# Performance work log

Measured on AMD Instinct MI355X. Metric: run time of the kernel, lower is better.

## Reference

```python
import jax, jax.numpy as jnp
import numpy as np

B, S, K, N, G = 4, 2048, 4096, 11008, 128


def setup_inputs() -> dict:
    key = jax.random.key(0)
    k1, k2, k3 = jax.random.split(key, 3)
    x = jax.random.normal(k1, (B, S, K), dtype=jnp.float32)
    # packed int4 GPTQ weights: (K/8, N) int32, 8 nibbles per int32
    qweight = jax.random.randint(k2, (K // 8, N), 0, 2147483647, dtype=jnp.int32)
    # per-group scales: (K/G, N), small positive values
    scales = jax.random.uniform(k3, (K // G, N), dtype=jnp.float32) * 0.01 + 0.001
    return {"x": x, "qweight": qweight, "scales": scales, "group_size": G}


def _dequantize(qweight, scales, group_size):
    shifts = jnp.arange(0, 32, 4, dtype=jnp.int32)          # [8]
    w = (qweight[:, None, :] >> shifts[None, :, None]) & 15  # (K/8, 8, N)
    k = w.shape[0] * 8
    w = w.reshape(k, -1)                                     # (K, N) in [0, 15]
    gidx = jnp.arange(k) // group_size                       # (K,)
    # symmetric int4 dequant with per-group, per-output-channel scale
    return (w.astype(scales.dtype) - 8.0) * scales[gidx]     # (K, N)


def reference(x, qweight, scales, group_size):
    Wf = _dequantize(qweight, scales, group_size)            # (K, N)
    return jnp.einsum('bsk,kn->bsn', x, Wf)                  # (B, S, N)
```

## Files before the change

kernel.cpp:

```cpp
#include <hip/hip_runtime.h>
#include <cstdint>
#include <cstddef>

#define M_DIM 8192
#define K_DIM 4096
#define N_DIM 11008
#define NT    (K_DIM / 64)

typedef short bf16x8 __attribute__((ext_vector_type(8)));
typedef float f32x4  __attribute__((ext_vector_type(4)));
typedef unsigned short us8 __attribute__((ext_vector_type(8)));

__device__ __forceinline__ unsigned short f2bf(float f) {
  unsigned int u = __float_as_uint(f);
  u += 0x7FFFu + ((u >> 16) & 1u);
  return (unsigned short)(u >> 16);
}

__global__ __launch_bounds__(256) void cvt_x_kernel(const float* __restrict__ x,
                                                    unsigned short* __restrict__ xb) {
  const int i = blockIdx.x * 256 + threadIdx.x;
  const float4* x4 = (const float4*)x;
  float4 a = x4[(size_t)i * 2];
  float4 b = x4[(size_t)i * 2 + 1];
  us8 o;
  o[0] = f2bf(a.x); o[1] = f2bf(a.y); o[2] = f2bf(a.z); o[3] = f2bf(a.w);
  o[4] = f2bf(b.x); o[5] = f2bf(b.y); o[6] = f2bf(b.z); o[7] = f2bf(b.w);
  *(us8*)(xb + (size_t)i * 8) = o;
}

__global__ __launch_bounds__(256) void dequant_kernel(const int* __restrict__ qw,
                                                      const float* __restrict__ sc,
                                                      unsigned short* __restrict__ wt) {
  const int n0 = blockIdx.x * 64;
  const int k0 = blockIdx.y * 64;
  const int g  = blockIdx.y >> 1;
  __shared__ unsigned short lds[64 * 64];
  const int t = threadIdx.x;
  {
    const int kk_l = t >> 5;
    const int n_l  = (t & 31) * 2;
    const int2  q2 = *(const int2*)&qw[(k0 / 8 + kk_l) * N_DIM + n0 + n_l];
    const float2 s2 = *(const float2*)&sc[g * N_DIM + n0 + n_l];
    us8 o0, o1;
#pragma unroll
    for (int j = 0; j < 8; ++j) {
      o0[j] = f2bf((float)(((q2.x >> (4 * j)) & 15) - 8) * s2.x);
      o1[j] = f2bf((float)(((q2.y >> (4 * j)) & 15) - 8) * s2.y);
    }
    *(us8*)&lds[(n_l    ) * 64 + kk_l * 8] = o0;
    *(us8*)&lds[(n_l + 1) * 64 + kk_l * 8] = o1;
  }
  __syncthreads();
#pragma unroll
  for (int it = 0; it < 2; ++it) {
    const int idx = t + it * 256;
    const int n_l = idx >> 3;
    const int ch  = (idx & 7) * 8;
    *(us8*)&wt[(size_t)(n0 + n_l) * K_DIM + k0 + ch] = *(const us8*)&lds[n_l * 64 + ch];
  }
}

__global__ __launch_bounds__(512, 2) void gemm_kernel(const unsigned short* __restrict__ A,
                                                      const unsigned short* __restrict__ Bt,
                                                      float* __restrict__ C) {
  __shared__ unsigned short lds[8][8192];
  const int t    = threadIdx.x;
  const int wave = t >> 6;
  const int lane = t & 63;
  const int l15  = lane & 15;
  const int wr   = wave >> 2;
  const int wc   = wave & 3;

  const int bid = blockIdx.x;
  const int wg  = (bid & 7) * 172 + (bid >> 3);
  const int m0  = (wg / 43) * 256;
  const int n0  = (wg % 43) * 256;

  const int sq = (t & 3) ^ ((t >> 3) & 3);
  const unsigned short* gA = A  + (size_t)(m0 + (t >> 2)) * K_DIM + sq * 8;
  const unsigned short* gB = Bt + (size_t)(n0 + (t >> 2)) * K_DIM + sq * 8;

  const int sxo   = ((lane >> 4) ^ ((l15 >> 1) & 3)) << 3;
  const int aoffA = (wr * 128 + l15) * 32 + sxo;
  const int aoffB = (wc * 64  + l15) * 32 + sxo;

  auto stage = [&](const unsigned short* gbase, unsigned short* reg, int h, int tk) {
#pragma unroll
    for (int j = 0; j < 2; ++j) {
      __builtin_amdgcn_global_load_lds(
          (const __attribute__((address_space(1))) unsigned int*)(gbase + (size_t)j * 128 * K_DIM + tk * 64 + h * 32),
          (__attribute__((address_space(3))) unsigned int*)(reg + j * 4096 + t * 8),
          16, 0, 0);
    }
  };

  f32x4 acc[8][4] = {};

  stage(gA, &lds[0][0], 0, 0);
  stage(gB, &lds[4][0], 0, 0);
  stage(gA, &lds[1][0], 1, 0);
  stage(gB, &lds[5][0], 1, 0);
  stage(gA, &lds[2][0], 0, 1);
  stage(gB, &lds[6][0], 0, 1);
  asm volatile("s_waitcnt vmcnt(4)" ::: "memory");
  __builtin_amdgcn_s_barrier();

#pragma unroll 1
  for (int tk = 0; tk < NT; ++tk) {
    const int p = tk & 1;
    const unsigned short* Ah0 = &lds[p * 2 + 0][0];
    const unsigned short* Ah1 = &lds[p * 2 + 1][0];
    const unsigned short* Bh0 = &lds[4 + p * 2 + 0][0];
    const unsigned short* Bh1 = &lds[4 + p * 2 + 1][0];
    unsigned short* stA1 = &lds[(p ^ 1) * 2 + 1][0];
    unsigned short* stB1 = &lds[4 + (p ^ 1) * 2 + 1][0];
    unsigned short* stA2 = &lds[p * 2 + 0][0];
    unsigned short* stB2 = &lds[4 + p * 2 + 0][0];

    bf16x8 a[4], b[4], a2[4];

#pragma unroll
    for (int i = 0; i < 4; ++i) a[i] = *(const bf16x8*)&Ah0[aoffA + i * 512];
#pragma unroll
    for (int i = 0; i < 4; ++i) b[i] = *(const bf16x8*)&Bh0[aoffB + i * 512];
    if (tk + 1 < NT) stage(gA, stA1, 1, tk + 1);
    __builtin_amdgcn_s_barrier();
    __builtin_amdgcn_s_setprio(1);
#pragma unroll
    for (int mi = 0; mi < 4; ++mi)
#pragma unroll
      for (int ni = 0; ni < 4; ++ni)
        acc[mi][ni] = __builtin_amdgcn_mfma_f32_16x16x32_bf16(a[mi], b[ni], acc[mi][ni], 0, 0, 0);
    __builtin_amdgcn_s_setprio(0);
    __builtin_amdgcn_s_barrier();

#pragma unroll
    for (int i = 0; i < 4; ++i) a2[i] = *(const bf16x8*)&Ah0[aoffA + (i + 4) * 512];
    if (tk + 1 < NT) stage(gB, stB1, 1, tk + 1);
    __builtin_amdgcn_s_barrier();
    __builtin_amdgcn_s_setprio(1);
#pragma unroll
    for (int mi = 0; mi < 4; ++mi)
#pragma unroll
      for (int ni = 0; ni < 4; ++ni)
        acc[mi + 4][ni] = __builtin_amdgcn_mfma_f32_16x16x32_bf16(a2[mi], b[ni], acc[mi + 4][ni], 0, 0, 0);
    __builtin_amdgcn_s_setprio(0);
    __builtin_amdgcn_s_barrier();

#pragma unroll
    for (int i = 0; i < 4; ++i) a[i] = *(const bf16x8*)&Ah1[aoffA + i * 512];
#pragma unroll
    for (int i = 0; i < 4; ++i) b[i] = *(const bf16x8*)&Bh1[aoffB + i * 512];
    if (tk + 2 < NT) stage(gA, stA2, 0, tk + 2);
    __builtin_amdgcn_s_barrier();
    __builtin_amdgcn_s_setprio(1);
#pragma unroll
    for (int mi = 0; mi < 4; ++mi)
#pragma unroll
      for (int ni = 0; ni < 4; ++ni)
        acc[mi][ni] = __builtin_amdgcn_mfma_f32_16x16x32_bf16(a[mi], b[ni], acc[mi][ni], 0, 0, 0);
    __builtin_amdgcn_s_setprio(0);
    __builtin_amdgcn_s_barrier();

#pragma unroll
    for (int i = 0; i < 4; ++i) a2[i] = *(const bf16x8*)&Ah1[aoffA + (i + 4) * 512];
    if (tk + 2 < NT) stage(gB, stB2, 0, tk + 2);
    __builtin_amdgcn_s_barrier();
    __builtin_amdgcn_s_setprio(1);
#pragma unroll
    for (int mi = 0; mi < 4; ++mi)
#pragma unroll
      for (int ni = 0; ni < 4; ++ni)
        acc[mi + 4][ni] = __builtin_amdgcn_mfma_f32_16x16x32_bf16(a2[mi], b[ni], acc[mi + 4][ni], 0, 0, 0);
    __builtin_amdgcn_s_setprio(0);
    if (tk + 2 < NT)      { asm volatile("s_waitcnt vmcnt(4)" ::: "memory"); }
    else if (tk + 1 < NT) { asm volatile("s_waitcnt vmcnt(0)" ::: "memory"); }
    __builtin_amdgcn_s_barrier();
  }

  const int cn = n0 + wc * 64 + l15;
  const int rm = m0 + wr * 128 + (lane >> 4) * 4;
#pragma unroll
  for (int mi = 0; mi < 8; ++mi)
#pragma unroll
    for (int ni = 0; ni < 4; ++ni)
#pragma unroll
      for (int r = 0; r < 4; ++r)
        C[(size_t)(rm + mi * 16 + r) * N_DIM + cn + ni * 16] = acc[mi][ni][r];
}

extern "C" void kernel_launch(void* const* d_in, const int* in_sizes, int n_in,
                              void* d_out, int out_size, void* d_ws, size_t ws_size,
                              hipStream_t stream) {
  const float* x  = (const float*)d_in[0];
  const int*   qw = (const int*)d_in[1];
  const float* sc = (const float*)d_in[2];
  float* out = (float*)d_out;

  unsigned short* xb = (unsigned short*)d_ws;
  unsigned short* wt = (unsigned short*)((char*)d_ws + (size_t)M_DIM * K_DIM * 2);

  cvt_x_kernel<<<dim3(M_DIM * K_DIM / (8 * 256)), dim3(256), 0, stream>>>(x, xb);
  dequant_kernel<<<dim3(N_DIM / 64, K_DIM / 64), dim3(256), 0, stream>>>(qw, sc, wt);
  gemm_kernel<<<dim3((N_DIM / 256) * (M_DIM / 256)), dim3(512), 0, stream>>>(xb, wt, out);
}
```

Baseline: 1.139 ms.

## Fuse int4 dequantization into GEMM B-tile staging, drop separate dequant kernel

Removes the standalone dequant kernel that materialized a bf16 transposed weight matrix. The GEMM now loads packed int4 words and scales into registers a stage early, then dequantizes them with an FMA and bf16 rounding and writes them into swizzled LDS B tiles. This cuts the launch and the round trip of the full bf16 weight matrix through HBM, and shrinks B global traffic to a quarter. In exchange, every tile block redoes the dequant ALU work (about 32 times over the M blocks), and the manual vmcnt waits become more intricate.

Measured after the change: 1.544 ms. 1.36x slower.

```diff
diff --git a/kernel.cpp b/kernel.cpp
--- a/kernel.cpp
+++ b/kernel.cpp
@@ -29,40 +29,26 @@
   *(us8*)(xb + (size_t)i * 8) = o;
 }
 
-__global__ __launch_bounds__(256) void dequant_kernel(const int* __restrict__ qw,
+union BU { us8 v; unsigned int u[4]; };
+__device__ __forceinline__ us8 dq8(unsigned int q, float s) {
+  const float b = -8.0f * s;
+  BU o;
+#pragma unroll
+  for (int j = 0; j < 4; ++j) {
+    float v0 = fmaf((float)((q >> (8 * j)) & 15u), s, b);
+    float v1 = fmaf((float)((q >> (8 * j + 4)) & 15u), s, b);
+    unsigned int u0 = __float_as_uint(v0);
+    unsigned int u1 = __float_as_uint(v1);
+    u0 += 0x7FFFu + ((u0 >> 16) & 1u);
+    u1 += 0x7FFFu + ((u1 >> 16) & 1u);
+    o.u[j] = (u0 >> 16) | (u1 & 0xFFFF0000u);
+  }
+  return o.v;
+}
+
+__global__ __launch_bounds__(512, 2) void gemm_kernel(const unsigned short* __restrict__ A,
+                                                      const int* __restrict__ qw,
                                                       const float* __restrict__ sc,
-                                                      unsigned short* __restrict__ wt) {
-  const int n0 = blockIdx.x * 64;
-  const int k0 = blockIdx.y * 64;
-  const int g  = blockIdx.y >> 1;
-  __shared__ unsigned short lds[64 * 64];
-  const int t = threadIdx.x;
-  {
-    const int kk_l = t >> 5;
-    const int n_l  = (t & 31) * 2;
-    const int2  q2 = *(const int2*)&qw[(k0 / 8 + kk_l) * N_DIM + n0 + n_l];
-    const float2 s2 = *(const float2*)&sc[g * N_DIM + n0 + n_l];
-    us8 o0, o1;
-#pragma unroll
-    for (int j = 0; j < 8; ++j) {
-      o0[j] = f2bf((float)(((q2.x >> (4 * j)) & 15) - 8) * s2.x);
-      o1[j] = f2bf((float)(((q2.y >> (4 * j)) & 15) - 8) * s2.y);
-    }
-    *(us8*)&lds[(n_l    ) * 64 + kk_l * 8] = o0;
-    *(us8*)&lds[(n_l + 1) * 64 + kk_l * 8] = o1;
-  }
-  __syncthreads();
-#pragma unroll
-  for (int it = 0; it < 2; ++it) {
-    const int idx = t + it * 256;
-    const int n_l = idx >> 3;
-    const int ch  = (idx & 7) * 8;
-    *(us8*)&wt[(size_t)(n0 + n_l) * K_DIM + k0 + ch] = *(const us8*)&lds[n_l * 64 + ch];
-  }
-}
-
-__global__ __launch_bounds__(512, 2) void gemm_kernel(const unsigned short* __restrict__ A,
-                                                      const unsigned short* __restrict__ Bt,
                                                       float* __restrict__ C) {
   __shared__ unsigned short lds[8][8192];
   const int t    = threadIdx.x;
@@ -78,33 +64,52 @@
   const int n0  = (wg % 43) * 256;
 
   const int sq = (t & 3) ^ ((t >> 3) & 3);
-  const unsigned short* gA = A  + (size_t)(m0 + (t >> 2)) * K_DIM + sq * 8;
-  const unsigned short* gB = Bt + (size_t)(n0 + (t >> 2)) * K_DIM + sq * 8;
+  const unsigned short* gA = A + (size_t)(m0 + (t >> 2)) * K_DIM + sq * 8;
+
+  const int n_l   = t >> 2;
+  const int c_log = t & 3;
+  const int* qp   = qw + n0 + n_l;
+  const float* sp = sc + n0 + n_l;
+  const int bo0 = n_l * 32 + ((c_log ^ ((n_l >> 1) & 3)) << 3);
+  const int bo1 = bo0 + 128 * 32;
 
   const int sxo   = ((lane >> 4) ^ ((l15 >> 1) & 3)) << 3;
   const int aoffA = (wr * 128 + l15) * 32 + sxo;
   const int aoffB = (wc * 64  + l15) * 32 + sxo;
 
-  auto stage = [&](const unsigned short* gbase, unsigned short* reg, int h, int tk) {
+  auto stageA = [&](unsigned short* reg, int h, int T) {
 #pragma unroll
     for (int j = 0; j < 2; ++j) {
       __builtin_amdgcn_global_load_lds(
-          (const __attribute__((address_space(1))) unsigned int*)(gbase + (size_t)j * 128 * K_DIM + tk * 64 + h * 32),
+          (const __attribute__((address_space(1))) unsigned int*)(gA + (size_t)j * 128 * K_DIM + T * 64 + h * 32),
           (__attribute__((address_space(3))) unsigned int*)(reg + j * 4096 + t * 8),
           16, 0, 0);
     }
   };
 
   f32x4 acc[8][4] = {};
-
-  stage(gA, &lds[0][0], 0, 0);
-  stage(gB, &lds[4][0], 0, 0);
-  stage(gA, &lds[1][0], 1, 0);
-  stage(gB, &lds[5][0], 1, 0);
-  stage(gA, &lds[2][0], 0, 1);
-  stage(gB, &lds[6][0], 0, 1);
-  asm volatile("s_waitcnt vmcnt(4)" ::: "memory");
-  __builtin_amdgcn_s_barrier();
+  unsigned int q0a, q0b; float s0a, s0b;
+  unsigned int q1a, q1b; float s1a, s1b;
+
+  stageA(&lds[0][0], 0, 0);
+  stageA(&lds[1][0], 1, 0);
+  {
+    unsigned int p00 = qp[(size_t)(0 + c_log) * N_DIM];
+    unsigned int p01 = qp[(size_t)(0 + c_log) * N_DIM + 128];
+    unsigned int p10 = qp[(size_t)(4 + c_log) * N_DIM];
+    unsigned int p11 = qp[(size_t)(4 + c_log) * N_DIM + 128];
+    float ss0 = sp[0], ss1 = sp[128];
+    *(us8*)&lds[4][bo0] = dq8(p00, ss0);
+    *(us8*)&lds[4][bo1] = dq8(p01, ss1);
+    *(us8*)&lds[5][bo0] = dq8(p10, ss0);
+    *(us8*)&lds[5][bo1] = dq8(p11, ss1);
+  }
+  stageA(&lds[2][0], 0, 1);
+  q0a = qp[(size_t)(8 + c_log) * N_DIM];
+  q0b = qp[(size_t)(8 + c_log) * N_DIM + 128];
+  s0a = sp[0];
+  s0b = sp[128];
+  __syncthreads();
 
 #pragma unroll 1
   for (int tk = 0; tk < NT; ++tk) {
@@ -113,10 +118,8 @@
     const unsigned short* Ah1 = &lds[p * 2 + 1][0];
     const unsigned short* Bh0 = &lds[4 + p * 2 + 0][0];
     const unsigned short* Bh1 = &lds[4 + p * 2 + 1][0];
-    unsigned short* stA1 = &lds[(p ^ 1) * 2 + 1][0];
-    unsigned short* stB1 = &lds[4 + (p ^ 1) * 2 + 1][0];
-    unsigned short* stA2 = &lds[p * 2 + 0][0];
-    unsigned short* stB2 = &lds[4 + p * 2 + 0][0];
+    unsigned short* wBh0 = &lds[4 + (p ^ 1) * 2 + 0][0];
+    unsigned short* wBh1 = &lds[4 + (p ^ 1) * 2 + 1][0];
 
     bf16x8 a[4], b[4], a2[4];
 
@@ -124,7 +127,7 @@
     for (int i = 0; i < 4; ++i) a[i] = *(const bf16x8*)&Ah0[aoffA + i * 512];
 #pragma unroll
     for (int i = 0; i < 4; ++i) b[i] = *(const bf16x8*)&Bh0[aoffB + i * 512];
-    if (tk + 1 < NT) stage(gA, stA1, 1, tk + 1);
+    if (tk + 1 < NT) stageA(&lds[(p ^ 1) * 2 + 1][0], 1, tk + 1);
     __builtin_amdgcn_s_barrier();
     __builtin_amdgcn_s_setprio(1);
 #pragma unroll
@@ -137,7 +140,15 @@
 
 #pragma unroll
     for (int i = 0; i < 4; ++i) a2[i] = *(const bf16x8*)&Ah0[aoffA + (i + 4) * 512];
-    if (tk + 1 < NT) stage(gB, stB1, 1, tk + 1);
+    if (tk + 1 < NT) {
+      q1a = qp[(size_t)((tk + 1) * 8 + 4 + c_log) * N_DIM];
+      q1b = qp[(size_t)((tk + 1) * 8 + 4 + c_log) * N_DIM + 128];
+      s1a = sp[(size_t)((tk + 1) >> 1) * N_DIM];
+      s1b = sp[(size_t)((tk + 1) >> 1) * N_DIM + 128];
+      asm volatile("s_waitcnt vmcnt(6)" ::: "memory");
+      *(us8*)&wBh0[bo0] = dq8(q0a, s0a);
+      *(us8*)&wBh0[bo1] = dq8(q0b, s0b);
+    }
     __builtin_amdgcn_s_barrier();
     __builtin_amdgcn_s_setprio(1);
 #pragma unroll
@@ -152,7 +163,13 @@
     for (int i = 0; i < 4; ++i) a[i] = *(const bf16x8*)&Ah1[aoffA + i * 512];
 #pragma unroll
     for (int i = 0; i < 4; ++i) b[i] = *(const bf16x8*)&Bh1[aoffB + i * 512];
-    if (tk + 2 < NT) stage(gA, stA2, 0, tk + 2);
+    if (tk + 2 < NT) stageA(&lds[p * 2 + 0][0], 0, tk + 2);
+    if (tk + 1 < NT) {
+      if (tk + 2 < NT) { asm volatile("s_waitcnt vmcnt(2)" ::: "memory"); }
+      else             { asm volatile("s_waitcnt vmcnt(0)" ::: "memory"); }
+      *(us8*)&wBh1[bo0] = dq8(q1a, s1a);
+      *(us8*)&wBh1[bo1] = dq8(q1b, s1b);
+    }
     __builtin_amdgcn_s_barrier();
     __builtin_amdgcn_s_setprio(1);
 #pragma unroll
@@ -165,7 +182,12 @@
 
 #pragma unroll
     for (int i = 0; i < 4; ++i) a2[i] = *(const bf16x8*)&Ah1[aoffA + (i + 4) * 512];
-    if (tk + 2 < NT) stage(gB, stB2, 0, tk + 2);
+    if (tk + 2 < NT) {
+      q0a = qp[(size_t)((tk + 2) * 8 + 0 + c_log) * N_DIM];
+      q0b = qp[(size_t)((tk + 2) * 8 + 0 + c_log) * N_DIM + 128];
+      s0a = sp[(size_t)((tk + 2) >> 1) * N_DIM];
+      s0b = sp[(size_t)((tk + 2) >> 1) * N_DIM + 128];
+    }
     __builtin_amdgcn_s_barrier();
     __builtin_amdgcn_s_setprio(1);
 #pragma unroll
@@ -174,8 +196,6 @@
       for (int ni = 0; ni < 4; ++ni)
         acc[mi + 4][ni] = __builtin_amdgcn_mfma_f32_16x16x32_bf16(a2[mi], b[ni], acc[mi + 4][ni], 0, 0, 0);
     __builtin_amdgcn_s_setprio(0);
-    if (tk + 2 < NT)      { asm volatile("s_waitcnt vmcnt(4)" ::: "memory"); }
-    else if (tk + 1 < NT) { asm volatile("s_waitcnt vmcnt(0)" ::: "memory"); }
     __builtin_amdgcn_s_barrier();
   }
 
@@ -199,9 +219,7 @@
   float* out = (float*)d_out;
 
   unsigned short* xb = (unsigned short*)d_ws;
-  unsigned short* wt = (unsigned short*)((char*)d_ws + (size_t)M_DIM * K_DIM * 2);
 
   cvt_x_kernel<<<dim3(M_DIM * K_DIM / (8 * 256)), dim3(256), 0, stream>>>(x, xb);
-  dequant_kernel<<<dim3(N_DIM / 64, K_DIM / 64), dim3(256), 0, stream>>>(qw, sc, wt);
-  gemm_kernel<<<dim3((N_DIM / 256) * (M_DIM / 256)), dim3(512), 0, stream>>>(xb, wt, out);
-}
+  gemm_kernel<<<dim3((N_DIM / 256) * (M_DIM / 256)), dim3(512), 0, stream>>>(xb, qw, sc, out);
+}
```
